# Optimization experiments

Hardware: AMD Instinct MI355X
Metric: run time of the kernel (lower is better)

Reference implementation:

```python
import jax, jax.numpy as jnp
import numpy as np

B, T, D, H = 2, 2048, 2048, 16
HD = D // H
SCALE = HD ** -0.5
NEG_INF = float('-inf')


def setup_inputs() -> dict:
    key = jax.random.key(0)
    ks = jax.random.split(key, 10)
    x = jax.random.normal(ks[0], (B, T, D), dtype=jnp.float32)
    # causal float mask: 0 on/below diagonal, -inf above (broadcast over B, H)
    causal = jnp.triu(jnp.ones((T, T), dtype=bool), k=1)
    mask = jnp.where(causal, NEG_INF, 0.0).astype(jnp.float32)[None, None]
    # xavier_uniform for [D, D]: bound = sqrt(6 / (D + D))
    bound = float(np.sqrt(6.0 / (D + D)))
    def xav(k):
        return jax.random.uniform(k, (D, D), jnp.float32, -bound, bound)
    wq, wk, wv, wo = xav(ks[1]), xav(ks[2]), xav(ks[3]), xav(ks[4])
    # biases: uniform_[0,1)
    bq = jax.random.uniform(ks[5], (D,), jnp.float32)
    bk = jax.random.uniform(ks[6], (D,), jnp.float32)
    bv = jax.random.uniform(ks[7], (D,), jnp.float32)
    bo = jax.random.uniform(ks[8], (D,), jnp.float32)
    return {"x": x, "mask": mask, "wq": wq, "bq": bq, "wk": wk, "bk": bk,
            "wv": wv, "bv": bv, "wo": wo, "bo": bo}


def reference(x, mask, wq, bq, wk, bk, wv, bv, wo, bo):
    b, t, d = x.shape
    def split_heads(y):  # [B,T,D] -> [B,H,T,HD]
        return y.reshape(b, t, H, HD).transpose(0, 2, 1, 3)
    q = split_heads(x @ wq.T + bq)
    k = split_heads(x @ wk.T + bk)
    v = split_heads(x @ wv.T + bv)
    scores = jnp.einsum('bhqd,bhkd->bhqk', q, k) * SCALE
    scores = jnp.where(mask == NEG_INF, NEG_INF, scores)
    attn = jax.nn.softmax(scores, axis=-1)
    out = jnp.einsum('bhqk,bhkd->bhqd', attn, v)  # [B,H,T,HD]
    out = out.transpose(0, 2, 1, 3).reshape(b, t, d)
    return out @ wo.T + bo
```

## Files before the change

### kernel.cpp

```cpp
#include <hip/hip_runtime.h>

typedef unsigned short u16;
typedef __bf16 bf16x8 __attribute__((ext_vector_type(8)));
typedef float f32x4 __attribute__((ext_vector_type(4)));

constexpr int B_ = 2, T_ = 2048, D_ = 2048, H_ = 16, HD_ = 128;
constexpr int MROWS = B_ * T_;
constexpr int KD = D_;
constexpr int ND = D_;
#define SL2E (0.08838834764831845f * 1.4426950408889634f)

__device__ __forceinline__ u16 f2bf(float f) {
  unsigned u = __float_as_uint(f);
  u += 0x7FFF + ((u >> 16) & 1);
  return (u16)(u >> 16);
}

__device__ __forceinline__ float fexp2(float x) { return __builtin_amdgcn_exp2f(x); }

__device__ __forceinline__ void async16(const void* g, void* l) {
  __builtin_amdgcn_global_load_lds((__attribute__((address_space(1))) void*)g,
                                   (__attribute__((address_space(3))) void*)l,
                                   16, 0, 0);
}

__global__ void cvt_kernel(const float* __restrict__ in, u16* __restrict__ out, int n) {
  int i = (blockIdx.x * blockDim.x + threadIdx.x) * 4;
  if (i >= n) return;
  const float4 v = *(const float4*)(in + i);
  ushort4 h;
  h.x = f2bf(v.x); h.y = f2bf(v.y); h.z = f2bf(v.z); h.w = f2bf(v.w);
  *(ushort4*)(out + i) = h;
}

__global__ void cvt4_kernel(const float* __restrict__ w0, const float* __restrict__ w1,
                            const float* __restrict__ w2, const float* __restrict__ w3,
                            u16* __restrict__ o0, u16* __restrict__ o1,
                            u16* __restrict__ o2, u16* __restrict__ o3, int n) {
  const float* in = blockIdx.y == 0 ? w0 : blockIdx.y == 1 ? w1 : blockIdx.y == 2 ? w2 : w3;
  u16* out = blockIdx.y == 0 ? o0 : blockIdx.y == 1 ? o1 : blockIdx.y == 2 ? o2 : o3;
  int i = (blockIdx.x * blockDim.x + threadIdx.x) * 4;
  if (i >= n) return;
  const float4 v = *(const float4*)(in + i);
  ushort4 h;
  h.x = f2bf(v.x); h.y = f2bf(v.y); h.z = f2bf(v.z); h.w = f2bf(v.w);
  *(ushort4*)(out + i) = h;
}

template <int MODE>
__device__ __forceinline__ void gemm_body(const u16* __restrict__ A,
                                          const u16* __restrict__ Bw,
                                          const float* __restrict__ bias,
                                          void* __restrict__ outp,
                                          u16* As, u16* Bs) {
  constexpr int BK = 32;
  const int tid = threadIdx.x;
  const int wave = tid >> 6;
  const int lane = tid & 63;
  const int quad = lane >> 4;
  const int l16 = lane & 15;
  const int wm = (wave >> 1) * 64;
  const int wn = (wave & 1) * 64;
  const int mBase = blockIdx.y * 128;
  const int nBase = blockIdx.x * 128;

  f32x4 acc[4][4] = {};

  const int srow = wave * 32 + (lane >> 2);
  const int soff = ((lane & 3) ^ ((lane >> 3) & 3)) * 8;
  const u16* Ag = A + (size_t)(mBase + srow) * KD + soff;
  const u16* Bg = Bw + (size_t)(nBase + srow) * KD + soff;
  u16* AsW0 = &As[(wave * 32) * BK];
  u16* AsW1 = &As[(wave * 32 + 16) * BK];
  u16* BsW0 = &Bs[(wave * 32) * BK];
  u16* BsW1 = &Bs[(wave * 32 + 16) * BK];

  const int sw = (quad ^ ((l16 >> 1) & 3)) * 8;

  for (int k0 = 0; k0 < KD; k0 += BK) {
    __syncthreads();
    async16(Ag + k0, AsW0);
    async16(Ag + 16 * KD + k0, AsW1);
    async16(Bg + k0, BsW0);
    async16(Bg + 16 * KD + k0, BsW1);
    __syncthreads();

    bf16x8 a[4], b[4];
#pragma unroll
    for (int i = 0; i < 4; i++)
      a[i] = *(const bf16x8*)&As[(wm + i * 16 + l16) * BK + sw];
#pragma unroll
    for (int j = 0; j < 4; j++)
      b[j] = *(const bf16x8*)&Bs[(wn + j * 16 + l16) * BK + sw];
#pragma unroll
    for (int i = 0; i < 4; i++)
#pragma unroll
      for (int j = 0; j < 4; j++)
        acc[i][j] = __builtin_amdgcn_mfma_f32_16x16x32_bf16(a[i], b[j], acc[i][j], 0, 0, 0);
  }

  float* outF = (float*)outp;
  u16* outH = (u16*)outp;
#pragma unroll
  for (int i = 0; i < 4; i++) {
#pragma unroll
    for (int j = 0; j < 4; j++) {
      const int col = nBase + wn + j * 16 + l16;
      const float bv = bias[col];
#pragma unroll
      for (int r = 0; r < 4; r++) {
        const int row = mBase + wm + i * 16 + quad * 4 + r;
        const float v = acc[i][j][r] + bv;
        if (MODE == 0) {
          outH[(size_t)row * ND + col] = f2bf(v);
        } else if (MODE == 1) {
          const int bb = row >> 11;
          const int t = row & (T_ - 1);
          const int h = col >> 7;
          const int d = col & (HD_ - 1);
          outH[(size_t)(((bb * H_ + h) << 7) + d) * T_ + t] = f2bf(v);
        } else {
          outF[(size_t)row * ND + col] = v;
        }
      }
    }
  }
}

__global__ __launch_bounds__(256) void gemm_qkv(const u16* __restrict__ A,
                                                const u16* __restrict__ Wq, const u16* __restrict__ Wk,
                                                const u16* __restrict__ Wv,
                                                const float* __restrict__ bq, const float* __restrict__ bk,
                                                const float* __restrict__ bv,
                                                u16* __restrict__ Qo, u16* __restrict__ Ko,
                                                u16* __restrict__ Vo) {
  __shared__ u16 As[128 * 32];
  __shared__ u16 Bs[128 * 32];
  const int z = blockIdx.z;
  const u16* Bw = z == 0 ? Wq : z == 1 ? Wk : Wv;
  const float* bias = z == 0 ? bq : z == 1 ? bk : bv;
  if (z == 2)
    gemm_body<1>(A, Bw, bias, (void*)Vo, As, Bs);
  else
    gemm_body<0>(A, Bw, bias, (void*)(z == 0 ? Qo : Ko), As, Bs);
}

__global__ __launch_bounds__(256) void gemm_out(const u16* __restrict__ A, const u16* __restrict__ Bw,
                                                const float* __restrict__ bias, float* __restrict__ outp) {
  __shared__ u16 As[128 * 32];
  __shared__ u16 Bs[128 * 32];
  gemm_body<2>(A, Bw, bias, (void*)outp, As, Bs);
}

constexpr int KSTR = 136;
constexpr int VSTR = 72;

__global__ __launch_bounds__(256) void attn_kernel(const u16* __restrict__ Q,
                                                   const u16* __restrict__ Kc,
                                                   const u16* __restrict__ Vt,
                                                   u16* __restrict__ O) {
  __shared__ u16 Ks[64 * KSTR];
  __shared__ u16 Vs[128 * VSTR];
  __shared__ u16 Ps[4 * 16 * VSTR];
  const int tid = threadIdx.x;
  const int wave = tid >> 6;
  const int lane = tid & 63;
  const int quad = lane >> 4;
  const int l16 = lane & 15;
  const int lo = blockIdx.x;
  const int hi = 31 - lo;
  const int bh = blockIdx.y;
  const int b = bh >> 4;
  const int h = bh & 15;

  const int tIdx[2] = {lo, hi};

  bf16x8 qf[2][4];
#pragma unroll
  for (int t = 0; t < 2; t++) {
    const u16* Qp = Q + (size_t)(b * T_ + tIdx[t] * 64 + wave * 16 + l16) * D_ + h * HD_;
#pragma unroll
    for (int kc = 0; kc < 4; kc++)
      qf[t][kc] = *(const bf16x8*)(Qp + kc * 32 + quad * 8);
  }

  f32x4 o[2][8] = {};
  float mrow[2], lrow[2];
#pragma unroll
  for (int t = 0; t < 2; t++) { mrow[t] = -__builtin_huge_valf(); lrow[t] = 0.f; }

  const u16* Kg = Kc + (size_t)(b * T_) * D_ + h * HD_;
  const u16* Vg = Vt + (size_t)((b * H_ + h) * HD_) * T_;
  u16* Pw = &Ps[wave * 16 * VSTR];

  for (int kt = 0; kt <= hi; kt++) {
    __syncthreads();
    {
      uint4 kv[4], vv[4];
      const int krow = tid >> 4, kc16 = tid & 15;
      const int vrow = tid >> 3, vc16 = tid & 7;
#pragma unroll
      for (int rr = 0; rr < 4; rr++)
        kv[rr] = *(const uint4*)(Kg + (size_t)(kt * 64 + rr * 16 + krow) * D_ + kc16 * 8);
#pragma unroll
      for (int rr = 0; rr < 4; rr++)
        vv[rr] = *(const uint4*)(Vg + (size_t)(rr * 32 + vrow) * T_ + kt * 64 + vc16 * 8);
#pragma unroll
      for (int rr = 0; rr < 4; rr++)
        *(uint4*)&Ks[(rr * 16 + krow) * KSTR + kc16 * 8] = kv[rr];
#pragma unroll
      for (int rr = 0; rr < 4; rr++)
        *(uint4*)&Vs[(rr * 32 + vrow) * VSTR + vc16 * 8] = vv[rr];
    }
    __syncthreads();

#pragma unroll
    for (int t = 0; t < 2; t++) {
      if (t == 0 && kt > lo) continue;

      f32x4 st[4];
#pragma unroll
      for (int nt = 0; nt < 4; nt++) {
        f32x4 a = {};
#pragma unroll
        for (int kc = 0; kc < 4; kc++) {
          bf16x8 kf = *(const bf16x8*)&Ks[(nt * 16 + l16) * KSTR + kc * 32 + quad * 8];
          a = __builtin_amdgcn_mfma_f32_16x16x32_bf16(kf, qf[t][kc], a, 0, 0, 0);
        }
        st[nt] = a;
      }

      const bool diag = (kt == tIdx[t]);
#pragma unroll
      for (int nt = 0; nt < 4; nt++)
#pragma unroll
        for (int r = 0; r < 4; r++) {
          float v = st[nt][r] * SL2E;
          if (diag) {
            const int kcol = nt * 16 + quad * 4 + r;
            const int qrow = wave * 16 + l16;
            if (kcol > qrow) v = -__builtin_huge_valf();
          }
          st[nt][r] = v;
        }

      float mx = st[0][0];
#pragma unroll
      for (int nt = 0; nt < 4; nt++)
#pragma unroll
        for (int r = 0; r < 4; r++) mx = fmaxf(mx, st[nt][r]);
      mx = fmaxf(mx, __shfl_xor(mx, 16));
      mx = fmaxf(mx, __shfl_xor(mx, 32));
      const float mnew = fmaxf(mrow[t], mx);
      const float alpha = fexp2(mrow[t] - mnew);
      mrow[t] = mnew;
      float sum = 0.f;
#pragma unroll
      for (int nt = 0; nt < 4; nt++)
#pragma unroll
        for (int r = 0; r < 4; r++) {
          const float p = fexp2(st[nt][r] - mnew);
          st[nt][r] = p;
          sum += p;
        }
      sum += __shfl_xor(sum, 16);
      sum += __shfl_xor(sum, 32);
      lrow[t] = lrow[t] * alpha + sum;

      float af[4];
#pragma unroll
      for (int r = 0; r < 4; r++) af[r] = __shfl(alpha, quad * 4 + r);
#pragma unroll
      for (int dt = 0; dt < 8; dt++)
#pragma unroll
        for (int r = 0; r < 4; r++)
          o[t][dt][r] *= af[r];

#pragma unroll
      for (int nt = 0; nt < 4; nt++) {
        ushort4 pk;
        pk.x = f2bf(st[nt][0]); pk.y = f2bf(st[nt][1]);
        pk.z = f2bf(st[nt][2]); pk.w = f2bf(st[nt][3]);
        *(ushort4*)&Pw[l16 * VSTR + nt * 16 + quad * 4] = pk;
      }

      bf16x8 pf[2];
#pragma unroll
      for (int kc = 0; kc < 2; kc++)
        pf[kc] = *(const bf16x8*)&Pw[l16 * VSTR + kc * 32 + quad * 8];
#pragma unroll
      for (int dt = 0; dt < 8; dt++) {
#pragma unroll
        for (int kc = 0; kc < 2; kc++) {
          bf16x8 vf = *(const bf16x8*)&Vs[(dt * 16 + l16) * VSTR + kc * 32 + quad * 8];
          o[t][dt] = __builtin_amdgcn_mfma_f32_16x16x32_bf16(pf[kc], vf, o[t][dt], 0, 0, 0);
        }
      }
    }
  }

#pragma unroll
  for (int t = 0; t < 2; t++) {
    float linv[4];
#pragma unroll
    for (int r = 0; r < 4; r++) linv[r] = 1.f / __shfl(lrow[t], quad * 4 + r);
#pragma unroll
    for (int dt = 0; dt < 8; dt++)
#pragma unroll
      for (int r = 0; r < 4; r++) {
        const int rowg = b * T_ + tIdx[t] * 64 + wave * 16 + quad * 4 + r;
        const int col = h * HD_ + dt * 16 + l16;
        O[(size_t)rowg * D_ + col] = f2bf(o[t][dt][r] * linv[r]);
      }
  }
}

extern "C" void kernel_launch(void* const* d_in, const int* in_sizes, int n_in,
                              void* d_out, int out_size, void* d_ws, size_t ws_size,
                              hipStream_t stream) {
  (void)in_sizes; (void)n_in; (void)out_size; (void)ws_size;
  const float* x  = (const float*)d_in[0];
  const float* wq = (const float*)d_in[2];
  const float* bq = (const float*)d_in[3];
  const float* wk = (const float*)d_in[4];
  const float* bk = (const float*)d_in[5];
  const float* wv = (const float*)d_in[6];
  const float* bv = (const float*)d_in[7];
  const float* wo = (const float*)d_in[8];
  const float* bo = (const float*)d_in[9];

  u16* ws  = (u16*)d_ws;
  u16* xb  = ws;
  u16* wqb = ws + 8388608;
  u16* wkb = ws + 12582912;
  u16* wvb = ws + 16777216;
  u16* wob = ws + 20971520;
  u16* Qb  = ws + 25165824;
  u16* Kb  = ws + 33554432;
  u16* Vtb = ws + 41943040;
  u16* Ob  = ws + 50331648;

  cvt_kernel<<<8192, 256, 0, stream>>>(x, xb, 8388608);
  cvt4_kernel<<<dim3(4096, 4), 256, 0, stream>>>(wq, wk, wv, wo, wqb, wkb, wvb, wob, 4194304);

  dim3 gg(ND / 128, MROWS / 128, 3);
  gemm_qkv<<<gg, 256, 0, stream>>>(xb, wqb, wkb, wvb, bq, bk, bv, Qb, Kb, Vtb);
  attn_kernel<<<dim3(16, B_ * H_), 256, 0, stream>>>(Qb, Kb, Vtb, Ob);
  gemm_out<<<dim3(ND / 128, MROWS / 128), 256, 0, stream>>>(Ob, wob, bo, (float*)d_out);
}
```

Measured before the change: 403.5 us.

## Double-buffer attention K/V tiles with async LDS loads and XOR swizzle

The attention kernel now stages K and V tiles straight from global memory into LDS with global_load_lds, into two buffers. The next tile is prefetched while the current one is consumed, and the second barrier per iteration is removed. Padded LDS strides are replaced by an XOR swizzle on 16-byte chunks to avoid bank conflicts. Launch bounds now request two blocks per CU. The aim is to hide global load latency and drop the register round-trip, at the cost of twice the LDS and a reliance on the barrier to wait for the async loads to finish.

```diff
diff --git a/kernel.cpp b/kernel.cpp
--- a/kernel.cpp
+++ b/kernel.cpp
@@ -152,16 +152,15 @@
   gemm_body<2>(A, Bw, bias, (void*)outp, As, Bs);
 }
 
-constexpr int KSTR = 136;
-constexpr int VSTR = 72;
-
-__global__ __launch_bounds__(256) void attn_kernel(const u16* __restrict__ Q,
-                                                   const u16* __restrict__ Kc,
-                                                   const u16* __restrict__ Vt,
-                                                   u16* __restrict__ O) {
-  __shared__ u16 Ks[64 * KSTR];
-  __shared__ u16 Vs[128 * VSTR];
-  __shared__ u16 Ps[4 * 16 * VSTR];
+constexpr int PSTR = 72;
+
+__global__ __launch_bounds__(256, 2) void attn_kernel(const u16* __restrict__ Q,
+                                                      const u16* __restrict__ Kc,
+                                                      const u16* __restrict__ Vt,
+                                                      u16* __restrict__ O) {
+  __shared__ u16 Ks[2][64 * 128];
+  __shared__ u16 Vs[2][128 * 64];
+  __shared__ u16 Ps[4 * 16 * PSTR];
   const int tid = threadIdx.x;
   const int wave = tid >> 6;
   const int lane = tid & 63;
@@ -191,28 +190,41 @@
 
   const u16* Kg = Kc + (size_t)(b * T_) * D_ + h * HD_;
   const u16* Vg = Vt + (size_t)((b * H_ + h) * HD_) * T_;
-  u16* Pw = &Ps[wave * 16 * VSTR];
+  u16* Pw = &Ps[wave * 16 * PSTR];
+  const int swz = (l16 & 7);
+
+  const u16* kgp[4];
+  int klo[4];
+  const u16* vgp[4];
+  int vlo[4];
+#pragma unroll
+  for (int c = 0; c < 4; c++) {
+    const int krl = wave * 16 + c * 4 + (lane >> 4);
+    const int kch = (lane & 15) ^ (krl & 7);
+    kgp[c] = Kg + (size_t)krl * D_ + kch * 8;
+    klo[c] = (wave * 16 + c * 4) * 128;
+    const int vrl = wave * 32 + c * 8 + (lane >> 3);
+    const int vch = (lane & 7) ^ (vrl & 7);
+    vgp[c] = Vg + (size_t)vrl * T_ + vch * 8;
+    vlo[c] = (wave * 32 + c * 8) * 64;
+  }
+
+#pragma unroll
+  for (int c = 0; c < 4; c++) async16(kgp[c], &Ks[0][klo[c]]);
+#pragma unroll
+  for (int c = 0; c < 4; c++) async16(vgp[c], &Vs[0][vlo[c]]);
 
   for (int kt = 0; kt <= hi; kt++) {
+    const int cur = kt & 1;
     __syncthreads();
-    {
-      uint4 kv[4], vv[4];
-      const int krow = tid >> 4, kc16 = tid & 15;
-      const int vrow = tid >> 3, vc16 = tid & 7;
-#pragma unroll
-      for (int rr = 0; rr < 4; rr++)
-        kv[rr] = *(const uint4*)(Kg + (size_t)(kt * 64 + rr * 16 + krow) * D_ + kc16 * 8);
-#pragma unroll
-      for (int rr = 0; rr < 4; rr++)
-        vv[rr] = *(const uint4*)(Vg + (size_t)(rr * 32 + vrow) * T_ + kt * 64 + vc16 * 8);
-#pragma unroll
-      for (int rr = 0; rr < 4; rr++)
-        *(uint4*)&Ks[(rr * 16 + krow) * KSTR + kc16 * 8] = kv[rr];
-#pragma unroll
-      for (int rr = 0; rr < 4; rr++)
-        *(uint4*)&Vs[(rr * 32 + vrow) * VSTR + vc16 * 8] = vv[rr];
+
+    if (kt < hi) {
+      const int nxt = cur ^ 1;
+#pragma unroll
+      for (int c = 0; c < 4; c++) async16(kgp[c] + (size_t)(kt + 1) * 64 * D_, &Ks[nxt][klo[c]]);
+#pragma unroll
+      for (int c = 0; c < 4; c++) async16(vgp[c] + (size_t)(kt + 1) * 64, &Vs[nxt][vlo[c]]);
     }
-    __syncthreads();
 
 #pragma unroll
     for (int t = 0; t < 2; t++) {
@@ -224,7 +236,8 @@
         f32x4 a = {};
 #pragma unroll
         for (int kc = 0; kc < 4; kc++) {
-          bf16x8 kf = *(const bf16x8*)&Ks[(nt * 16 + l16) * KSTR + kc * 32 + quad * 8];
+          const int pos = (kc * 4 + quad) ^ swz;
+          bf16x8 kf = *(const bf16x8*)&Ks[cur][(nt * 16 + l16) * 128 + pos * 8];
           a = __builtin_amdgcn_mfma_f32_16x16x32_bf16(kf, qf[t][kc], a, 0, 0, 0);
         }
         st[nt] = a;
@@ -281,18 +294,19 @@
         ushort4 pk;
         pk.x = f2bf(st[nt][0]); pk.y = f2bf(st[nt][1]);
         pk.z = f2bf(st[nt][2]); pk.w = f2bf(st[nt][3]);
-        *(ushort4*)&Pw[l16 * VSTR + nt * 16 + quad * 4] = pk;
+        *(ushort4*)&Pw[l16 * PSTR + nt * 16 + quad * 4] = pk;
       }
 
       bf16x8 pf[2];
 #pragma unroll
       for (int kc = 0; kc < 2; kc++)
-        pf[kc] = *(const bf16x8*)&Pw[l16 * VSTR + kc * 32 + quad * 8];
+        pf[kc] = *(const bf16x8*)&Pw[l16 * PSTR + kc * 32 + quad * 8];
 #pragma unroll
       for (int dt = 0; dt < 8; dt++) {
 #pragma unroll
         for (int kc = 0; kc < 2; kc++) {
-          bf16x8 vf = *(const bf16x8*)&Vs[(dt * 16 + l16) * VSTR + kc * 32 + quad * 8];
+          const int pos = (kc * 4 + quad) ^ swz;
+          bf16x8 vf = *(const bf16x8*)&Vs[cur][(dt * 16 + l16) * 64 + pos * 8];
           o[t][dt] = __builtin_amdgcn_mfma_f32_16x16x32_bf16(pf[kc], vf, o[t][dt], 0, 0, 0);
         }
       }
```

Measured after the change: 395.0 us. 1.02x faster.
